# Kernel tuning notes

Measured on AMD Instinct MI355X. Metric: run time of the kernel, lower is better.

Reference implementation:

```python
import jax, jax.numpy as jnp
import numpy as np

S = 7          # grid size
B = 2          # boxes per cell
C = 20         # classes (last dim = B*5 + C = 30)
IMG = 448.0    # img_size
GAMMA_COORD = 5.0
GAMMA_NOOBJ = 0.5
BS = 8192


def setup_inputs() -> dict:
    key = jax.random.key(0)
    k1, k2, k3 = jax.random.split(key, 3)
    output = jax.random.uniform(k1, (BS, S, S, B * 5 + C), dtype=jnp.float32)
    target = jax.random.uniform(k2, (BS, S, S, B * 5 + C), dtype=jnp.float32)
    grid_mask_obj = jax.random.randint(k3, (BS, S, S), 0, 2).astype(jnp.int32)
    return {"output": output, "target": target, "grid_mask_obj": grid_mask_obj}


def _decode_xyxy(t):
    """t: (bs,S,S,B*5) raw boxes -> pixel-space corner boxes x1,y1,x2,y2, each (bs,S,S,B)."""
    boxes = t.reshape(t.shape[:3] + (B, 5))
    cell = 1.0 / S
    gx = (jnp.arange(S, dtype=t.dtype) * cell)[None, None, :, None]  # varies along m (col)
    gy = (jnp.arange(S, dtype=t.dtype) * cell)[None, :, None, None]  # varies along n (row)
    x = (boxes[..., 0] * cell + gx) * IMG
    y = (boxes[..., 1] * cell + gy) * IMG
    w = boxes[..., 2] * IMG
    h = boxes[..., 3] * IMG
    return x - w / 2, y - h / 2, x + w / 2, y + h / 2


def _yolo_loss(output, target, grid_mask_obj):
    bs = output.shape[0]
    obj = (grid_mask_obj != 0).astype(output.dtype)          # (bs,S,S)

    boxes_o = output[..., : B * 5].reshape(output.shape[:3] + (B, 5))
    boxes_t = target[..., : B * 5].reshape(target.shape[:3] + (B, 5))

    # --- IoU of each predicted box vs target box 0 (matches box_iou(...)[:, 0]) ---
    ox1, oy1, ox2, oy2 = _decode_xyxy(output[..., : B * 5])   # (bs,S,S,B)
    tx1, ty1, tx2, ty2 = _decode_xyxy(target[..., : B * 5])
    tx1, ty1, tx2, ty2 = tx1[..., :1], ty1[..., :1], tx2[..., :1], ty2[..., :1]  # target box 0
    iw = jnp.clip(jnp.minimum(ox2, tx2) - jnp.maximum(ox1, tx1), 0.0)
    ih = jnp.clip(jnp.minimum(oy2, ty2) - jnp.maximum(oy1, ty1), 0.0)
    inter = iw * ih
    area_o = (ox2 - ox1) * (oy2 - oy1)
    area_t = (tx2 - tx1) * (ty2 - ty1)
    ious = inter / (area_o + area_t - inter)                  # (bs,S,S,B)

    max_iou = jnp.max(ious, axis=-1)                          # (bs,S,S)
    max_id = jnp.argmax(ious, axis=-1)                        # (bs,S,S)
    onehot = jax.nn.one_hot(max_id, B, dtype=output.dtype)
    obj_ij_mask = onehot * obj[..., None]
    obj_ij_ious = onehot * max_iou[..., None] * obj[..., None]

    box_id_reg = jnp.argmax(obj_ij_mask, axis=-1)             # (bs,S,S)
    box_id_conf = jnp.argmax(obj_ij_ious, axis=-1)

    sel_o = jnp.take_along_axis(boxes_o, box_id_reg[..., None, None], axis=3)[..., 0, :]
    sel_t = jnp.take_along_axis(boxes_t, box_id_reg[..., None, None], axis=3)[..., 0, :]
    xy_loss = jnp.sum(obj * jnp.sum((sel_o[..., 0:2] - sel_t[..., 0:2]) ** 2, axis=-1))
    wh_loss = jnp.sum(obj * jnp.sum((jnp.sqrt(sel_o[..., 2:4]) - jnp.sqrt(sel_t[..., 2:4])) ** 2, axis=-1))

    # --- confidence loss (obj cells): predicted conf vs matched IoU ---
    conf_o = boxes_o[..., 4]                                  # (bs,S,S,B)
    conf_t = boxes_t[..., 4]
    sel_c = jnp.take_along_axis(conf_o, box_id_conf[..., None], axis=3)[..., 0]
    sel_iou = jnp.take_along_axis(obj_ij_ious, box_id_conf[..., None], axis=3)[..., 0]
    c_loss_obj = jnp.sum(obj * (sel_c - sel_iou) ** 2)

    # --- confidence loss (noobj cells): all B boxes ---
    c_loss_noobj = jnp.sum((1.0 - obj)[..., None] * (conf_o - conf_t) ** 2)

    # --- class probability loss (obj cells) ---
    cls_loss = jnp.sum(obj[..., None] * (output[..., B * 5:] - target[..., B * 5:]) ** 2)

    return (GAMMA_COORD * (xy_loss + wh_loss)
            + c_loss_obj
            + GAMMA_NOOBJ * c_loss_noobj
            + cls_loss) / bs


def reference(output, target, grid_mask_obj):
    return _yolo_loss(output, target, grid_mask_obj)
```

## Files before the change

kernel.cpp:

```cpp
#include <hip/hip_runtime.h>


constexpr int   S_      = 7;
constexpr float IMG_    = 448.0f;
constexpr float CELLW_  = 1.0f / 7.0f;
constexpr float INV_BS_ = 1.0f / 8192.0f;

__global__ __launch_bounds__(256) void yolo_loss_kernel(
    const float* __restrict__ outp, const float* __restrict__ tgtp,
    const int* __restrict__ maskp, float* __restrict__ res, int ncell)
{
    int idx = blockIdx.x * blockDim.x + threadIdx.x;
    float acc = 0.0f;

    if (idx < ncell) {
        const float2* po = reinterpret_cast<const float2*>(outp) + (size_t)idx * 15;
        const float2* pt = reinterpret_cast<const float2*>(tgtp) + (size_t)idx * 15;
        float o[30], t[30];
#pragma unroll
        for (int k = 0; k < 15; ++k) {
            float2 v = po[k]; o[2*k] = v.x; o[2*k+1] = v.y;
            float2 w = pt[k]; t[2*k] = w.x; t[2*k+1] = w.y;
        }
        int m = maskp[idx];

        int rem = idx % 49;
        float gx = (float)(rem % 7) * CELLW_;
        float gy = (float)(rem / 7) * CELLW_;

        float tx = (t[0] * CELLW_ + gx) * IMG_;
        float ty = (t[1] * CELLW_ + gy) * IMG_;
        float tw = t[2] * IMG_, th = t[3] * IMG_;
        float tx1 = tx - tw * 0.5f, tx2 = tx + tw * 0.5f;
        float ty1 = ty - th * 0.5f, ty2 = ty + th * 0.5f;
        float area_t = (tx2 - tx1) * (ty2 - ty1);

        float iou[2];
#pragma unroll
        for (int b = 0; b < 2; ++b) {
            float b0 = (b == 0) ? o[0] : o[5];
            float b1 = (b == 0) ? o[1] : o[6];
            float b2 = (b == 0) ? o[2] : o[7];
            float b3 = (b == 0) ? o[3] : o[8];
            float x = (b0 * CELLW_ + gx) * IMG_;
            float y = (b1 * CELLW_ + gy) * IMG_;
            float w = b2 * IMG_, h = b3 * IMG_;
            float x1 = x - w * 0.5f, x2 = x + w * 0.5f;
            float y1 = y - h * 0.5f, y2 = y + h * 0.5f;
            float iw = fmaxf(fminf(x2, tx2) - fmaxf(x1, tx1), 0.0f);
            float ih = fmaxf(fminf(y2, ty2) - fmaxf(y1, ty1), 0.0f);
            float inter = iw * ih;
            float area_o = (x2 - x1) * (y2 - y1);
            iou[b] = inter / (area_o + area_t - inter);
        }

        int   max_id  = (iou[1] > iou[0]) ? 1 : 0;
        float max_iou = fmaxf(iou[0], iou[1]);

        float so0 = max_id ? o[5] : o[0];
        float so1 = max_id ? o[6] : o[1];
        float so2 = max_id ? o[7] : o[2];
        float so3 = max_id ? o[8] : o[3];
        float st0 = max_id ? t[5] : t[0];
        float st1 = max_id ? t[6] : t[1];
        float st2 = max_id ? t[7] : t[2];
        float st3 = max_id ? t[8] : t[3];

        float dxy0 = so0 - st0, dxy1 = so1 - st1;
        float xy_loss = dxy0 * dxy0 + dxy1 * dxy1;

        float dwh0 = sqrtf(so2) - sqrtf(st2);
        float dwh1 = sqrtf(so3) - sqrtf(st3);
        float wh_loss = dwh0 * dwh0 + dwh1 * dwh1;

        int   id_conf = (max_iou > 0.0f) ? max_id : 0;
        float sel_c   = id_conf ? o[9] : o[4];
        float sel_iou = (id_conf == max_id) ? max_iou : 0.0f;
        float dcf     = sel_c - sel_iou;
        float c_obj   = dcf * dcf;

        float cls = 0.0f;
#pragma unroll
        for (int k = 10; k < 30; ++k) {
            float d = o[k] - t[k];
            cls += d * d;
        }

        float dn0 = o[4] - t[4], dn1 = o[9] - t[9];
        float c_noobj = dn0 * dn0 + dn1 * dn1;

        acc = m ? (5.0f * (xy_loss + wh_loss) + c_obj + cls)
                : (0.5f * c_noobj);
    }

#pragma unroll
    for (int off = 32; off > 0; off >>= 1)
        acc += __shfl_down(acc, off);

    __shared__ float wsum[4];
    int lane = threadIdx.x & 63;
    int wid  = threadIdx.x >> 6;
    if (lane == 0) wsum[wid] = acc;
    __syncthreads();
    if (threadIdx.x == 0) {
        float bsum = wsum[0] + wsum[1] + wsum[2] + wsum[3];
        atomicAdd(res, bsum * INV_BS_);
    }
}

extern "C" void kernel_launch(void* const* d_in, const int* in_sizes, int n_in,
                              void* d_out, int out_size, void* d_ws, size_t ws_size,
                              hipStream_t stream) {
    const float* outp = (const float*)d_in[0];
    const float* tgtp = (const float*)d_in[1];
    const int*   mask = (const int*)d_in[2];
    float*       res  = (float*)d_out;

    int ncell = in_sizes[2];

    hipMemsetAsync(d_out, 0, sizeof(float), stream);

    int threads = 256;
    int blocks  = (ncell + threads - 1) / threads;
    yolo_loss_kernel<<<blocks, threads, 0, stream>>>(outp, tgtp, mask, res, ncell);
}
```

Before: 125.0 us.

## Coalesce cell loads through LDS and fold class loss into load loop

Threads now read the output and target arrays cooperatively in contiguous float2 strides instead of each thread reading its own 120-byte cell. Class-probability differences are accumulated during the load loop, and only the 10 box fields per cell are staged in shared memory for the per-cell IoU and box logic. This is meant to fix the strided uncoalesced global access of the old per-thread layout. The trade-off is extra LDS traffic and a barrier, plus dropping the tail bounds check, which assumes ncell is a multiple of 256 (true for 8192*49).

```diff
diff --git a/kernel.cpp b/kernel.cpp
--- a/kernel.cpp
+++ b/kernel.cpp
@@ -1,39 +1,68 @@
 #include <hip/hip_runtime.h>
 
 
-constexpr int   S_      = 7;
+constexpr float CELLW_  = 1.0f / 7.0f;
 constexpr float IMG_    = 448.0f;
-constexpr float CELLW_  = 1.0f / 7.0f;
 constexpr float INV_BS_ = 1.0f / 8192.0f;
 
 __global__ __launch_bounds__(256) void yolo_loss_kernel(
     const float* __restrict__ outp, const float* __restrict__ tgtp,
-    const int* __restrict__ maskp, float* __restrict__ res, int ncell)
+    const int* __restrict__ maskp, float* __restrict__ res)
 {
-    int idx = blockIdx.x * blockDim.x + threadIdx.x;
+    __shared__ int   lmask[256];
+    __shared__ float lo[256 * 11];
+    __shared__ float lt[256 * 11];
+
+    const int tid   = threadIdx.x;
+    const int cell0 = blockIdx.x * 256;
+
+    lmask[tid] = maskp[cell0 + tid];
+    __syncthreads();
+
+    const float2* po = reinterpret_cast<const float2*>(outp) + (size_t)cell0 * 15;
+    const float2* pt = reinterpret_cast<const float2*>(tgtp) + (size_t)cell0 * 15;
+
     float acc = 0.0f;
 
-    if (idx < ncell) {
-        const float2* po = reinterpret_cast<const float2*>(outp) + (size_t)idx * 15;
-        const float2* pt = reinterpret_cast<const float2*>(tgtp) + (size_t)idx * 15;
-        float o[30], t[30];
+    int c  = (2 * tid) / 30;
+    int ch = (2 * tid) - c * 30;
+
 #pragma unroll
-        for (int k = 0; k < 15; ++k) {
-            float2 v = po[k]; o[2*k] = v.x; o[2*k+1] = v.y;
-            float2 w = pt[k]; t[2*k] = w.x; t[2*k+1] = w.y;
+    for (int k = 0; k < 15; ++k) {
+        const int j = tid + 256 * k;
+        float2 vo = po[j];
+        float2 vt = pt[j];
+        if (ch < 10) {
+            lo[c * 11 + ch]     = vo.x;
+            lo[c * 11 + ch + 1] = vo.y;
+            lt[c * 11 + ch]     = vt.x;
+            lt[c * 11 + ch + 1] = vt.y;
+        } else {
+            float dx = vo.x - vt.x;
+            float dy = vo.y - vt.y;
+            float add = dx * dx + dy * dy;
+            acc += lmask[c] ? add : 0.0f;
         }
-        int m = maskp[idx];
+        ch += 2; c += 17;
+        if (ch >= 30) { ch -= 30; c += 1; }
+    }
+    __syncthreads();
 
-        int rem = idx % 49;
-        float gx = (float)(rem % 7) * CELLW_;
-        float gy = (float)(rem / 7) * CELLW_;
+    {
+        const float* o = &lo[tid * 11];
+        const float* t = &lt[tid * 11];
+        const int    m = lmask[tid];
 
-        float tx = (t[0] * CELLW_ + gx) * IMG_;
-        float ty = (t[1] * CELLW_ + gy) * IMG_;
-        float tw = t[2] * IMG_, th = t[3] * IMG_;
-        float tx1 = tx - tw * 0.5f, tx2 = tx + tw * 0.5f;
-        float ty1 = ty - th * 0.5f, ty2 = ty + th * 0.5f;
-        float area_t = (tx2 - tx1) * (ty2 - ty1);
+        const int rem = (cell0 + tid) % 49;
+        const float gx = (float)(rem % 7) * CELLW_;
+        const float gy = (float)(rem / 7) * CELLW_;
+
+        const float tx = (t[0] * CELLW_ + gx) * IMG_;
+        const float ty = (t[1] * CELLW_ + gy) * IMG_;
+        const float tw = t[2] * IMG_, th = t[3] * IMG_;
+        const float tx1 = tx - tw * 0.5f, tx2 = tx + tw * 0.5f;
+        const float ty1 = ty - th * 0.5f, ty2 = ty + th * 0.5f;
+        const float area_t = (tx2 - tx1) * (ty2 - ty1);
 
         float iou[2];
 #pragma unroll
@@ -54,43 +83,36 @@
             iou[b] = inter / (area_o + area_t - inter);
         }
 
-        int   max_id  = (iou[1] > iou[0]) ? 1 : 0;
-        float max_iou = fmaxf(iou[0], iou[1]);
+        const int   max_id  = (iou[1] > iou[0]) ? 1 : 0;
+        const float max_iou = fmaxf(iou[0], iou[1]);
 
-        float so0 = max_id ? o[5] : o[0];
-        float so1 = max_id ? o[6] : o[1];
-        float so2 = max_id ? o[7] : o[2];
-        float so3 = max_id ? o[8] : o[3];
-        float st0 = max_id ? t[5] : t[0];
-        float st1 = max_id ? t[6] : t[1];
-        float st2 = max_id ? t[7] : t[2];
-        float st3 = max_id ? t[8] : t[3];
+        const float so0 = max_id ? o[5] : o[0];
+        const float so1 = max_id ? o[6] : o[1];
+        const float so2 = max_id ? o[7] : o[2];
+        const float so3 = max_id ? o[8] : o[3];
+        const float st0 = max_id ? t[5] : t[0];
+        const float st1 = max_id ? t[6] : t[1];
+        const float st2 = max_id ? t[7] : t[2];
+        const float st3 = max_id ? t[8] : t[3];
 
-        float dxy0 = so0 - st0, dxy1 = so1 - st1;
-        float xy_loss = dxy0 * dxy0 + dxy1 * dxy1;
+        const float dxy0 = so0 - st0, dxy1 = so1 - st1;
+        const float xy_loss = dxy0 * dxy0 + dxy1 * dxy1;
 
-        float dwh0 = sqrtf(so2) - sqrtf(st2);
-        float dwh1 = sqrtf(so3) - sqrtf(st3);
-        float wh_loss = dwh0 * dwh0 + dwh1 * dwh1;
+        const float dwh0 = sqrtf(so2) - sqrtf(st2);
+        const float dwh1 = sqrtf(so3) - sqrtf(st3);
+        const float wh_loss = dwh0 * dwh0 + dwh1 * dwh1;
 
-        int   id_conf = (max_iou > 0.0f) ? max_id : 0;
-        float sel_c   = id_conf ? o[9] : o[4];
-        float sel_iou = (id_conf == max_id) ? max_iou : 0.0f;
-        float dcf     = sel_c - sel_iou;
-        float c_obj   = dcf * dcf;
+        const int   id_conf = (max_iou > 0.0f) ? max_id : 0;
+        const float sel_c   = id_conf ? o[9] : o[4];
+        const float sel_iou = (id_conf == max_id) ? max_iou : 0.0f;
+        const float dcf     = sel_c - sel_iou;
+        const float c_obj   = dcf * dcf;
 
-        float cls = 0.0f;
-#pragma unroll
-        for (int k = 10; k < 30; ++k) {
-            float d = o[k] - t[k];
-            cls += d * d;
-        }
+        const float dn0 = o[4] - t[4], dn1 = o[9] - t[9];
+        const float c_noobj = dn0 * dn0 + dn1 * dn1;
 
-        float dn0 = o[4] - t[4], dn1 = o[9] - t[9];
-        float c_noobj = dn0 * dn0 + dn1 * dn1;
-
-        acc = m ? (5.0f * (xy_loss + wh_loss) + c_obj + cls)
-                : (0.5f * c_noobj);
+        acc += m ? (5.0f * (xy_loss + wh_loss) + c_obj)
+                 : (0.5f * c_noobj);
     }
 
 #pragma unroll
@@ -98,8 +120,8 @@
         acc += __shfl_down(acc, off);
 
     __shared__ float wsum[4];
-    int lane = threadIdx.x & 63;
-    int wid  = threadIdx.x >> 6;
+    const int lane = threadIdx.x & 63;
+    const int wid  = threadIdx.x >> 6;
     if (lane == 0) wsum[wid] = acc;
     __syncthreads();
     if (threadIdx.x == 0) {
@@ -116,11 +138,11 @@
     const int*   mask = (const int*)d_in[2];
     float*       res  = (float*)d_out;
 
-    int ncell = in_sizes[2];
+    const int ncell = in_sizes[2];
 
     hipMemsetAsync(d_out, 0, sizeof(float), stream);
 
-    int threads = 256;
-    int blocks  = (ncell + threads - 1) / threads;
-    yolo_loss_kernel<<<blocks, threads, 0, stream>>>(outp, tgtp, mask, res, ncell);
+    const int threads = 256;
+    const int blocks  = ncell / threads;
+    yolo_loss_kernel<<<blocks, threads, 0, stream>>>(outp, tgtp, mask, res);
 }
```

Result: slower. 135.1 us (+8.1%).
